# Performance work log

Measured on AMD Instinct MI355X. Metric: run time of the kernel, lower is better.

Reference implementation:

```python
import jax, jax.numpy as jnp
import numpy as np

NEG_INF = -1e30  # value the original assigns to exactly-zero scores


def setup_inputs() -> dict:
    key = jax.random.key(0)
    kq, kk, kv = jax.random.split(key, 3)
    B, Lq, Lk, d = 16, 4096, 4096, 64
    queries = jax.random.normal(kq, (B, Lq, d), dtype=jnp.float32)
    keys = jax.random.normal(kk, (B, Lk, d), dtype=jnp.float32)
    values = jax.random.normal(kv, (B, Lk, d), dtype=jnp.float32)
    return {"queries": queries, "keys": keys, "values": values}


def reference(queries, keys, values):
    d = queries.shape[-1]
    # [B, Lq, Lk] full score matrix, scaled
    scores = jnp.einsum("bqd,bkd->bqk", queries, keys) / jnp.sqrt(
        jnp.asarray(d, dtype=queries.dtype)
    )
    # zero-score masking: scores[scores == 0] = -1e30
    scores = jnp.where(scores == 0, jnp.asarray(NEG_INF, dtype=scores.dtype), scores)
    attn = jax.nn.softmax(scores, axis=-1)
    # dropout prob is 0.0 -> identity
    return jnp.einsum("bqk,bkd->bqd", attn, values)
```

## Files before the change

### kernel.cpp

```cpp
#include <hip/hip_runtime.h>
#include <hip/hip_bf16.h>
#include <math.h>

typedef __attribute__((ext_vector_type(4))) float f32x4;
typedef __attribute__((ext_vector_type(8))) short s16x8;

#define B_    16
#define L_    4096
#define D_    64
#define QB    128
#define KVB   64
#define NT    (L_ / KVB)

#define QSCALE 0.18033688011112042f
#define THR    8.0f

__device__ __forceinline__ unsigned short f2bf(float x) {
  union { float f; unsigned u; } v; v.f = x;
  unsigned r = v.u + 0x7FFFu + ((v.u >> 16) & 1u);
  return (unsigned short)(r >> 16);
}

__device__ __forceinline__ int swz(int x) {
  return ((x & 7) ^ ((x >> 3) & 7)) << 4;
}

__device__ __forceinline__ void gload_lds16(const void* g, void* l) {
  __builtin_amdgcn_global_load_lds(
      (const __attribute__((address_space(1))) void*)g,
      (__attribute__((address_space(3))) void*)l, 16, 0, 0);
}

__device__ __forceinline__ unsigned cvtpk_bf16(float lo, float hi) {
  unsigned r;
  asm("v_cvt_pk_bf16_f32 %0, %1, %2" : "=v"(r) : "v"(lo), "v"(hi));
  return r;
}

__device__ __forceinline__ void pl32_swap(unsigned& a, unsigned& b) {
#if __has_builtin(__builtin_amdgcn_permlane32_swap)
  auto r = __builtin_amdgcn_permlane32_swap(a, b, false, false);
  a = r[0]; b = r[1];
#else
  asm volatile("v_permlane32_swap_b32 %0, %1" : "+v"(a), "+v"(b));
#endif
}

__device__ __forceinline__ void pl16_swap(unsigned& a, unsigned& b) {
#if __has_builtin(__builtin_amdgcn_permlane16_swap)
  auto r = __builtin_amdgcn_permlane16_swap(a, b, false, false);
  a = r[0]; b = r[1];
#else
  asm volatile("v_permlane16_swap_b32 %0, %1" : "+v"(a), "+v"(b));
#endif
}

__device__ __forceinline__ float fexp2(float x) {
#if __has_builtin(__builtin_amdgcn_exp2f)
  return __builtin_amdgcn_exp2f(x);
#else
  return exp2f(x);
#endif
}

__global__ __launch_bounds__(256) void prep_kv4(
    const float* __restrict__ Kg, const float* __restrict__ Vg,
    unsigned short* __restrict__ Kw, unsigned short* __restrict__ Vw) {
  __shared__ unsigned short vim[KVB * D_];
  const int tid = threadIdx.x;
  int blk = blockIdx.x;
  if (blk < B_ * NT) {
    const float* src = Kg + (size_t)blk * (KVB * D_);
    char* dst = (char*)(Kw + (size_t)blk * (KVB * D_));
#pragma unroll
    for (int c = 0; c < 2; ++c) {
      const int ch  = tid + c * 256;
      const int key = ch >> 3;
      const int seg = ch & 7;
      const float* p = src + key * D_ + seg * 8;
      f32x4 x0 = *(const f32x4*)p;
      f32x4 x1 = *(const f32x4*)(p + 4);
      union { s16x8 v; unsigned w[4]; } t_;
      t_.w[0] = cvtpk_bf16(x0[0], x0[1]);
      t_.w[1] = cvtpk_bf16(x0[2], x0[3]);
      t_.w[2] = cvtpk_bf16(x1[0], x1[1]);
      t_.w[3] = cvtpk_bf16(x1[2], x1[3]);
      *(s16x8*)(dst + ((key * 128 + seg * 16) ^ swz(key))) = t_.v;
    }
  } else {
    blk -= B_ * NT;
    const int skey2 = (tid >> 3) * 2;
    const int sdseg = tid & 7;
    const float* vp0 = Vg + ((size_t)blk * KVB + skey2) * D_ + sdseg * 8;
    char* vimc = (char*)vim;
    f32x4 v0 = *(const f32x4*)(vp0);
    f32x4 v1 = *(const f32x4*)(vp0 + 4);
    f32x4 v2 = *(const f32x4*)(vp0 + D_);
    f32x4 v3 = *(const f32x4*)(vp0 + D_ + 4);
#pragma unroll
    for (int u = 0; u < 2; ++u) {
#pragma unroll
      for (int i = 0; i < 4; ++i) {
        const int d = sdseg * 8 + u * 4 + i;
        unsigned pk = cvtpk_bf16(u ? v1[i] : v0[i], u ? v3[i] : v2[i]);
        *(unsigned*)(vimc + ((d * 128 + skey2 * 2) ^ swz(d))) = pk;
      }
    }
    __syncthreads();
    char* vout = (char*)(Vw + (size_t)blk * (KVB * D_));
#pragma unroll
    for (int c = 0; c < 2; ++c) {
      const int off = c * 4096 + tid * 16;
      *(s16x8*)(vout + off) = *(const s16x8*)(vimc + off);
    }
  }
}

__global__ __launch_bounds__(256, 2) void attn_fwd5(
    const float* __restrict__ Qg, const unsigned short* __restrict__ Kw,
    const unsigned short* __restrict__ Vw, float* __restrict__ Og) {
  __shared__ unsigned short Ks[2][KVB * D_];
  __shared__ unsigned short Vs[2][KVB * D_];

  const int tid  = threadIdx.x;
  const int wv   = tid >> 6;
  const int lane = tid & 63;
  const int rl   = lane & 15;
  const int kb   = lane >> 4;
  const int kb4  = kb * 4;

  const int blk = blockIdx.x;
  const int b   = blk >> 5;
  const int qt  = blk & 31;

  const float* qbase = Qg + ((size_t)b * L_ + qt * QB + wv * 32) * D_;
  s16x8 aq0[2], aq1[2];
#pragma unroll
  for (int qh = 0; qh < 2; ++qh) {
    const float* qrow_p = qbase + (qh * 16 + rl) * D_;
#pragma unroll
    for (int h = 0; h < 2; ++h) {
      const float* p = qrow_p + h * 32 + kb * 8;
      f32x4 x0 = *(const f32x4*)p;
      f32x4 x1 = *(const f32x4*)(p + 4);
      union { s16x8 v; unsigned w[4]; } t_;
      t_.w[0] = cvtpk_bf16(x0[0] * QSCALE, x0[1] * QSCALE);
      t_.w[1] = cvtpk_bf16(x0[2] * QSCALE, x0[3] * QSCALE);
      t_.w[2] = cvtpk_bf16(x1[0] * QSCALE, x1[1] * QSCALE);
      t_.w[3] = cvtpk_bf16(x1[2] * QSCALE, x1[3] * QSCALE);
      if (qh == 0) aq0[h] = t_.v; else aq1[h] = t_.v;
    }
  }

  int offA[4], offB[4];
#pragma unroll
  for (int t = 0; t < 4; ++t) {
    const int row  = t * 16 + rl;
    const int base = row * 128 + kb * 16;
    offA[t] = base ^ swz(row);
    offB[t] = (base + 64) ^ swz(row);
  }

  f32x4 oacc0[4], oacc1[4];
#pragma unroll
  for (int t = 0; t < 4; ++t) {
    oacc0[t] = (f32x4){0.f, 0.f, 0.f, 0.f};
    oacc1[t] = (f32x4){0.f, 0.f, 0.f, 0.f};
  }
  float m0 = -3.0e38f, m1 = -3.0e38f, l0 = 0.f, l1 = 0.f;

  char* ks0 = (char*)(&Ks[0][0]);
  char* vs0 = (char*)(&Vs[0][0]);
  const int woff = wv * 2048;
  const char* kt = (const char*)(Kw + (size_t)b * L_ * D_) + woff + lane * 16;
  const char* vt = (const char*)(Vw + (size_t)b * L_ * D_) + woff + lane * 16;

  auto compute = [&](const char* kbase, const char* vbase) {
    f32x4 s0[4], s1[4];
    __builtin_amdgcn_s_setprio(1);
#pragma unroll
    for (int t = 0; t < 4; ++t) {
      s16x8 k0 = *(const s16x8*)(kbase + offA[t]);
      s16x8 k1 = *(const s16x8*)(kbase + offB[t]);
      f32x4 a = (f32x4){0.f, 0.f, 0.f, 0.f};
      f32x4 c = (f32x4){0.f, 0.f, 0.f, 0.f};
      a = __builtin_amdgcn_mfma_f32_16x16x32_bf16(k0, aq0[0], a, 0, 0, 0);
      c = __builtin_amdgcn_mfma_f32_16x16x32_bf16(k0, aq1[0], c, 0, 0, 0);
      a = __builtin_amdgcn_mfma_f32_16x16x32_bf16(k1, aq0[1], a, 0, 0, 0);
      c = __builtin_amdgcn_mfma_f32_16x16x32_bf16(k1, aq1[1], c, 0, 0, 0);
      s0[t] = a; s1[t] = c;
    }
    __builtin_amdgcn_s_setprio(0);

    float x0 = fmaxf(fmaxf(s0[0][0], s0[0][1]), fmaxf(s0[0][2], s0[0][3]));
    float x1 = fmaxf(fmaxf(s0[1][0], s0[1][1]), fmaxf(s0[1][2], s0[1][3]));
    float x2 = fmaxf(fmaxf(s0[2][0], s0[2][1]), fmaxf(s0[2][2], s0[2][3]));
    float x3 = fmaxf(fmaxf(s0[3][0], s0[3][1]), fmaxf(s0[3][2], s0[3][3]));
    float mx0 = fmaxf(fmaxf(x0, x1), fmaxf(x2, x3));
    float y0 = fmaxf(fmaxf(s1[0][0], s1[0][1]), fmaxf(s1[0][2], s1[0][3]));
    float y1 = fmaxf(fmaxf(s1[1][0], s1[1][1]), fmaxf(s1[1][2], s1[1][3]));
    float y2 = fmaxf(fmaxf(s1[2][0], s1[2][1]), fmaxf(s1[2][2], s1[2][3]));
    float y3 = fmaxf(fmaxf(s1[3][0], s1[3][1]), fmaxf(s1[3][2], s1[3][3]));
    float mx1 = fmaxf(fmaxf(y0, y1), fmaxf(y2, y3));

    if (__any((mx0 > m0 + THR) || (mx1 > m1 + THR))) {
      float r0 = fmaxf(mx0, __shfl_xor(mx0, 16));
      r0 = fmaxf(r0, __shfl_xor(r0, 32));
      float r1 = fmaxf(mx1, __shfl_xor(mx1, 16));
      r1 = fmaxf(r1, __shfl_xor(r1, 32));
      const float n0 = fmaxf(m0, r0);
      const float n1 = fmaxf(m1, r1);
      const float al0 = fexp2(m0 - n0);
      const float al1 = fexp2(m1 - n1);
      m0 = n0; m1 = n1;
      l0 *= al0; l1 *= al1;
#pragma unroll
      for (int j = 0; j < 4; ++j) {
        const float b0 = __shfl(al0, kb4 + j);
        const float b1 = __shfl(al1, kb4 + j);
#pragma unroll
        for (int t = 0; t < 4; ++t) {
          oacc0[t][j] *= b0;
          oacc1[t][j] *= b1;
        }
      }
    }

    unsigned W0[4][2], W1[4][2];
    float rs0 = 0.f, rs1 = 0.f;
#pragma unroll
    for (int t = 0; t < 4; ++t) {
      const float e0 = fexp2(s0[t][0] - m0);
      const float e1 = fexp2(s0[t][1] - m0);
      const float e2 = fexp2(s0[t][2] - m0);
      const float e3 = fexp2(s0[t][3] - m0);
      rs0 += (e0 + e1) + (e2 + e3);
      W0[t][0] = cvtpk_bf16(e0, e1);
      W0[t][1] = cvtpk_bf16(e2, e3);
      const float f0 = fexp2(s1[t][0] - m1);
      const float f1 = fexp2(s1[t][1] - m1);
      const float f2 = fexp2(s1[t][2] - m1);
      const float f3 = fexp2(s1[t][3] - m1);
      rs1 += (f0 + f1) + (f2 + f3);
      W1[t][0] = cvtpk_bf16(f0, f1);
      W1[t][1] = cvtpk_bf16(f2, f3);
    }
    l0 += rs0; l1 += rs1;

    union { s16x8 v; unsigned w[4]; } A00, A01, A10, A11;
#pragma unroll
    for (int u = 0; u < 2; ++u) {
      { unsigned x = W0[0][u], y = W0[1][u];
        pl32_swap(x, y); pl16_swap(x, y);
        A00.w[u] = x; A00.w[u + 2] = y; }
      { unsigned x = W0[2][u], y = W0[3][u];
        pl32_swap(x, y); pl16_swap(x, y);
        A01.w[u] = x; A01.w[u + 2] = y; }
      { unsigned x = W1[0][u], y = W1[1][u];
        pl32_swap(x, y); pl16_swap(x, y);
        A10.w[u] = x; A10.w[u + 2] = y; }
      { unsigned x = W1[2][u], y = W1[3][u];
        pl32_swap(x, y); pl16_swap(x, y);
        A11.w[u] = x; A11.w[u + 2] = y; }
    }

    __builtin_amdgcn_s_setprio(1);
#pragma unroll
    for (int t = 0; t < 4; ++t) {
      s16x8 bv0 = *(const s16x8*)(vbase + offA[t]);
      s16x8 bv1 = *(const s16x8*)(vbase + offB[t]);
      f32x4 a = oacc0[t];
      f32x4 c = oacc1[t];
      a = __builtin_amdgcn_mfma_f32_16x16x32_bf16(A00.v, bv0, a, 0, 0, 0);
      c = __builtin_amdgcn_mfma_f32_16x16x32_bf16(A10.v, bv0, c, 0, 0, 0);
      a = __builtin_amdgcn_mfma_f32_16x16x32_bf16(A01.v, bv1, a, 0, 0, 0);
      c = __builtin_amdgcn_mfma_f32_16x16x32_bf16(A11.v, bv1, c, 0, 0, 0);
      oacc0[t] = a; oacc1[t] = c;
    }
    __builtin_amdgcn_s_setprio(0);
  };

  gload_lds16(kt,        ks0 + woff);
  gload_lds16(kt + 1024, ks0 + woff + 1024);
  gload_lds16(vt,        vs0 + woff);
  gload_lds16(vt + 1024, vs0 + woff + 1024);
  kt += 8192; vt += 8192;
  __syncthreads();

  int boff = 0;
  for (int kv = 0; kv < NT - 1; ++kv) {
    const int nb = boff ^ 8192;
    gload_lds16(kt,        ks0 + nb + woff);
    gload_lds16(kt + 1024, ks0 + nb + woff + 1024);
    gload_lds16(vt,        vs0 + nb + woff);
    gload_lds16(vt + 1024, vs0 + nb + woff + 1024);
    kt += 8192; vt += 8192;

    compute(ks0 + boff, vs0 + boff);
    __syncthreads();
    boff = nb;
  }
  compute(ks0 + boff, vs0 + boff);

  float t0 = l0 + __shfl_xor(l0, 16);
  t0 += __shfl_xor(t0, 32);
  float t1 = l1 + __shfl_xor(l1, 16);
  t1 += __shfl_xor(t1, 32);
  const float v0i = 1.0f / t0;
  const float v1i = 1.0f / t1;

  float* ob = Og + ((size_t)b * L_ + qt * QB + wv * 32 + kb4) * D_;
#pragma unroll
  for (int j = 0; j < 4; ++j) {
    const float i0 = __shfl(v0i, kb4 + j);
    const float i1 = __shfl(v1i, kb4 + j);
    float* r0 = ob + (size_t)j * D_;
    float* r1 = r0 + 16 * D_;
#pragma unroll
    for (int t = 0; t < 4; ++t) {
      r0[t * 16 + rl] = oacc0[t][j] * i0;
      r1[t * 16 + rl] = oacc1[t][j] * i1;
    }
  }
}

__global__ __launch_bounds__(256) void attn_fwd_fb(
    const float* __restrict__ Qg, const float* __restrict__ Kg,
    const float* __restrict__ Vg, float* __restrict__ Og) {
  __shared__ unsigned short Ksf[KVB * D_];
  __shared__ unsigned short Vsf[KVB * D_];
  __shared__ unsigned short Psf[4][16 * KVB];

  const int tid  = threadIdx.x;
  const int wv   = tid >> 6;
  const int lane = tid & 63;
  const int rl   = lane & 15;
  const int kb   = lane >> 4;

  const int blk = blockIdx.x;
  const int b   = blk / (L_ / 64);
  const int qt  = blk % (L_ / 64);

  const float* qrow_p = Qg + ((size_t)b * L_ + qt * 64 + wv * 16 + rl) * D_;
  s16x8 aq[2];
#pragma unroll
  for (int h = 0; h < 2; ++h) {
    const float* p = qrow_p + h * 32 + kb * 8;
    f32x4 x0 = *(const f32x4*)p;
    f32x4 x1 = *(const f32x4*)(p + 4);
    s16x8 w;
#pragma unroll
    for (int i = 0; i < 4; ++i) {
      w[i]     = (short)f2bf(x0[i] * QSCALE);
      w[i + 4] = (short)f2bf(x1[i] * QSCALE);
    }
    aq[h] = w;
  }

  f32x4 oacc[4];
  float m_r[4], l_r[4];
#pragma unroll
  for (int t = 0; t < 4; ++t) oacc[t] = (f32x4){0.f, 0.f, 0.f, 0.f};
#pragma unroll
  for (int j = 0; j < 4; ++j) { m_r[j] = -3.0e38f; l_r[j] = 0.f; }

  const float* kb_p = Kg + (size_t)b * L_ * D_;
  const float* vb_p = Vg + (size_t)b * L_ * D_;
  const int skey2 = (tid >> 3) * 2;
  const int sdseg = tid & 7;

  char* ksc = (char*)Ksf;
  char* vsc = (char*)Vsf;
  char* psc = (char*)(Psf[wv]);

  for (int kv = 0; kv < L_; kv += KVB) {
    __syncthreads();
    {
      const float* kp0 = kb_p + (size_t)(kv + skey2) * D_ + sdseg * 8;
      const float* vp0 = vb_p + (size_t)(kv + skey2) * D_ + sdseg * 8;
#pragma unroll
      for (int q2 = 0; q2 < 2; ++q2) {
        const int key = skey2 + q2;
        f32x4 a0 = *(const f32x4*)(kp0 + q2 * D_);
        f32x4 a1 = *(const f32x4*)(kp0 + q2 * D_ + 4);
        s16x8 w;
#pragma unroll
        for (int i = 0; i < 4; ++i) {
          w[i]     = (short)f2bf(a0[i]);
          w[i + 4] = (short)f2bf(a1[i]);
        }
        *(s16x8*)(ksc + ((key * 128 + sdseg * 16) ^ swz(key))) = w;
      }
      f32x4 v0 = *(const f32x4*)(vp0);
      f32x4 v1 = *(const f32x4*)(vp0 + 4);
      f32x4 v2 = *(const f32x4*)(vp0 + D_);
      f32x4 v3 = *(const f32x4*)(vp0 + D_ + 4);
#pragma unroll
      for (int u = 0; u < 2; ++u) {
#pragma unroll
        for (int i = 0; i < 4; ++i) {
          const int d = sdseg * 8 + u * 4 + i;
          unsigned lo = (unsigned)f2bf(u ? v1[i] : v0[i]);
          unsigned hi = (unsigned)f2bf(u ? v3[i] : v2[i]);
          *(unsigned*)(vsc + ((d * 128 + skey2 * 2) ^ swz(d))) = lo | (hi << 16);
        }
      }
    }
    __syncthreads();

    f32x4 s[4];
#pragma unroll
    for (int t = 0; t < 4; ++t) {
      const int key  = t * 16 + rl;
      const int base = key * 128 + kb * 16;
      s16x8 b0 = *(const s16x8*)(ksc + ((base)      ^ swz(key)));
      s16x8 b1 = *(const s16x8*)(ksc + ((base + 64) ^ swz(key)));
      f32x4 acc = (f32x4){0.f, 0.f, 0.f, 0.f};
      acc = __builtin_amdgcn_mfma_f32_16x16x32_bf16(aq[0], b0, acc, 0, 0, 0);
      acc = __builtin_amdgcn_mfma_f32_16x16x32_bf16(aq[1], b1, acc, 0, 0, 0);
      s[t] = acc;
    }

    float alpha[4];
#pragma unroll
    for (int j = 0; j < 4; ++j) {
      float mx = fmaxf(fmaxf(s[0][j], s[1][j]), fmaxf(s[2][j], s[3][j]));
      mx = fmaxf(mx, __shfl_xor(mx, 1));
      mx = fmaxf(mx, __shfl_xor(mx, 2));
      mx = fmaxf(mx, __shfl_xor(mx, 4));
      mx = fmaxf(mx, __shfl_xor(mx, 8));
      const float mn = fmaxf(m_r[j], mx);
      alpha[j] = fexp2(m_r[j] - mn);
      m_r[j]   = mn;
    }

    float rs[4] = {0.f, 0.f, 0.f, 0.f};
#pragma unroll
    for (int t = 0; t < 4; ++t)
#pragma unroll
      for (int j = 0; j < 4; ++j) {
        const float p = fexp2(s[t][j] - m_r[j]);
        rs[j] += p;
        const int row = kb * 4 + j;
        *(unsigned short*)(psc + ((row * 128 + (t * 16 + rl) * 2) ^ swz(row))) = f2bf(p);
      }
#pragma unroll
    for (int j = 0; j < 4; ++j) l_r[j] = l_r[j] * alpha[j] + rs[j];

#pragma unroll
    for (int t = 0; t < 4; ++t)
#pragma unroll
      for (int j = 0; j < 4; ++j) oacc[t][j] *= alpha[j];

    s16x8 ap[2];
#pragma unroll
    for (int h = 0; h < 2; ++h) {
      const int base = rl * 128 + h * 64 + kb * 16;
      ap[h] = *(const s16x8*)(psc + (base ^ swz(rl)));
    }
#pragma unroll
    for (int t = 0; t < 4; ++t) {
      const int d    = t * 16 + rl;
      const int base = d * 128 + kb * 16;
      s16x8 bv0 = *(const s16x8*)(vsc + ((base)      ^ swz(d)));
      s16x8 bv1 = *(const s16x8*)(vsc + ((base + 64) ^ swz(d)));
      f32x4 acc = oacc[t];
      acc = __builtin_amdgcn_mfma_f32_16x16x32_bf16(ap[0], bv0, acc, 0, 0, 0);
      acc = __builtin_amdgcn_mfma_f32_16x16x32_bf16(ap[1], bv1, acc, 0, 0, 0);
      oacc[t] = acc;
    }
  }

  float inv[4];
#pragma unroll
  for (int j = 0; j < 4; ++j) {
    float r = l_r[j];
    r += __shfl_xor(r, 1);
    r += __shfl_xor(r, 2);
    r += __shfl_xor(r, 4);
    r += __shfl_xor(r, 8);
    inv[j] = 1.0f / r;
  }
  float* op = Og + ((size_t)b * L_ + qt * 64 + wv * 16 + kb * 4) * D_;
#pragma unroll
  for (int j = 0; j < 4; ++j)
#pragma unroll
    for (int t = 0; t < 4; ++t)
      op[(size_t)j * D_ + t * 16 + rl] = oacc[t][j] * inv[j];
}

extern "C" void kernel_launch(void* const* d_in, const int* in_sizes, int n_in,
                              void* d_out, int out_size, void* d_ws, size_t ws_size,
                              hipStream_t stream) {
  (void)in_sizes; (void)n_in; (void)out_size;
  const float* Q = (const float*)d_in[0];
  const float* K = (const float*)d_in[1];
  const float* V = (const float*)d_in[2];
  float* O = (float*)d_out;

  const size_t need = (size_t)2 * B_ * L_ * D_ * sizeof(unsigned short);
  if (d_ws != nullptr && ws_size >= need) {
    unsigned short* Kw = (unsigned short*)d_ws;
    unsigned short* Vw = Kw + (size_t)B_ * L_ * D_;
    prep_kv4<<<dim3(2 * B_ * NT), 256, 0, stream>>>(K, V, Kw, Vw);
    attn_fwd5<<<dim3(B_ * (L_ / QB)), 256, 0, stream>>>(Q, Kw, Vw, O);
  } else {
    attn_fwd_fb<<<dim3(B_ * (L_ / 64)), 256, 0, stream>>>(Q, K, V, O);
  }
}
```

Measured before the change: 193.5 us.

## Deepen K/V prefetch to a four-stage LDS ring with vmcnt-gated barriers

Replaces the double-buffered K/V LDS pipeline with a four-slot ring that keeps three tiles in flight. Each iteration waits on vmcnt for only the oldest tile, then does a single barrier before issuing the next load and computing. This is meant to hide more global-to-LDS latency and drop one barrier per iteration. LDS per block doubles to 64 KB, which may limit how many blocks fit per CU, and correctness rests on the hand-written vmcnt counts.

```diff
diff --git a/kernel.cpp b/kernel.cpp
--- a/kernel.cpp
+++ b/kernel.cpp
@@ -116,11 +116,11 @@
   }
 }
 
-__global__ __launch_bounds__(256, 2) void attn_fwd5(
+__global__ __launch_bounds__(256, 2) void attn_fwd6(
     const float* __restrict__ Qg, const unsigned short* __restrict__ Kw,
     const unsigned short* __restrict__ Vw, float* __restrict__ Og) {
-  __shared__ unsigned short Ks[2][KVB * D_];
-  __shared__ unsigned short Vs[2][KVB * D_];
+  __shared__ unsigned short Ks[4][KVB * D_];
+  __shared__ unsigned short Vs[4][KVB * D_];
 
   const int tid  = threadIdx.x;
   const int wv   = tid >> 6;
@@ -174,6 +174,16 @@
   const int woff = wv * 2048;
   const char* kt = (const char*)(Kw + (size_t)b * L_ * D_) + woff + lane * 16;
   const char* vt = (const char*)(Vw + (size_t)b * L_ * D_) + woff + lane * 16;
+
+  auto issue = [&](int bi) {
+    char* kd = ks0 + bi * 8192 + woff;
+    char* vd = vs0 + bi * 8192 + woff;
+    gload_lds16(kt,        kd);
+    gload_lds16(kt + 1024, kd + 1024);
+    gload_lds16(vt,        vd);
+    gload_lds16(vt + 1024, vd + 1024);
+    kt += 8192; vt += 8192;
+  };
 
   auto compute = [&](const char* kbase, const char* vbase) {
     f32x4 s0[4], s1[4];
@@ -280,27 +290,34 @@
     __builtin_amdgcn_s_setprio(0);
   };
 
-  gload_lds16(kt,        ks0 + woff);
-  gload_lds16(kt + 1024, ks0 + woff + 1024);
-  gload_lds16(vt,        vs0 + woff);
-  gload_lds16(vt + 1024, vs0 + woff + 1024);
-  kt += 8192; vt += 8192;
-  __syncthreads();
-
-  int boff = 0;
-  for (int kv = 0; kv < NT - 1; ++kv) {
-    const int nb = boff ^ 8192;
-    gload_lds16(kt,        ks0 + nb + woff);
-    gload_lds16(kt + 1024, ks0 + nb + woff + 1024);
-    gload_lds16(vt,        vs0 + nb + woff);
-    gload_lds16(vt + 1024, vs0 + nb + woff + 1024);
-    kt += 8192; vt += 8192;
-
-    compute(ks0 + boff, vs0 + boff);
-    __syncthreads();
-    boff = nb;
-  }
-  compute(ks0 + boff, vs0 + boff);
+  issue(0); issue(1); issue(2);
+
+  for (int i = 0; i < NT - 3; ++i) {
+    asm volatile("s_waitcnt vmcnt(8)" ::: "memory");
+    __builtin_amdgcn_sched_barrier(0);
+    __builtin_amdgcn_s_barrier();
+    __builtin_amdgcn_sched_barrier(0);
+    issue((i + 3) & 3);
+    compute(ks0 + (i & 3) * 8192, vs0 + (i & 3) * 8192);
+  }
+
+  asm volatile("s_waitcnt vmcnt(8)" ::: "memory");
+  __builtin_amdgcn_sched_barrier(0);
+  __builtin_amdgcn_s_barrier();
+  __builtin_amdgcn_sched_barrier(0);
+  compute(ks0 + ((NT - 3) & 3) * 8192, vs0 + ((NT - 3) & 3) * 8192);
+
+  asm volatile("s_waitcnt vmcnt(4)" ::: "memory");
+  __builtin_amdgcn_sched_barrier(0);
+  __builtin_amdgcn_s_barrier();
+  __builtin_amdgcn_sched_barrier(0);
+  compute(ks0 + ((NT - 2) & 3) * 8192, vs0 + ((NT - 2) & 3) * 8192);
+
+  asm volatile("s_waitcnt vmcnt(0)" ::: "memory");
+  __builtin_amdgcn_sched_barrier(0);
+  __builtin_amdgcn_s_barrier();
+  __builtin_amdgcn_sched_barrier(0);
+  compute(ks0 + ((NT - 1) & 3) * 8192, vs0 + ((NT - 1) & 3) * 8192);
 
   float t0 = l0 + __shfl_xor(l0, 16);
   t0 += __shfl_xor(t0, 32);
@@ -503,7 +520,7 @@
     unsigned short* Kw = (unsigned short*)d_ws;
     unsigned short* Vw = Kw + (size_t)B_ * L_ * D_;
     prep_kv4<<<dim3(2 * B_ * NT), 256, 0, stream>>>(K, V, Kw, Vw);
-    attn_fwd5<<<dim3(B_ * (L_ / QB)), 256, 0, stream>>>(Q, Kw, Vw, O);
+    attn_fwd6<<<dim3(B_ * (L_ / QB)), 256, 0, stream>>>(Q, Kw, Vw, O);
   } else {
     attn_fwd_fb<<<dim3(B_ * (L_ / 64)), 256, 0, stream>>>(Q, K, V, O);
   }
```

Result: no change. 191.1 us (-1.2%).
